# Kernel tuning notes

Hardware: AMD Instinct MI355X
Metric: run time of the kernel (lower is better)

Reference implementation:

```python
import jax, jax.numpy as jnp
import numpy as np

B, S, D = 4, 2048, 1024

def setup_inputs() -> dict:
    key = jax.random.key(0)
    k1, k2, k3, k4 = jax.random.split(key, 4)
    scale = 1.0 / np.sqrt(D)  # roughly glorot-like magnitude for weights
    return {
        "inputs": jax.random.normal(k1, (B, S, D), dtype=jnp.float32),
        "W_query": jax.random.normal(k2, (D, D), dtype=jnp.float32) * scale,
        "W_key": jax.random.normal(k3, (D, D), dtype=jnp.float32) * scale,
        "W_value": jax.random.normal(k4, (D, D), dtype=jnp.float32) * scale,
    }

def reference(inputs, W_query, W_key, W_value):
    # QKV projections: [B,S,D] @ [D,D]
    q = jnp.einsum('bsd,de->bse', inputs, W_query)
    k = jnp.einsum('bsd,de->bse', inputs, W_key)
    v = jnp.einsum('bsd,de->bse', inputs, W_value)
    # Unscaled attention scores [B,S,S] (source applies no 1/sqrt(d))
    score = jnp.einsum('bqd,bkd->bqk', q, k)
    weights = jax.nn.softmax(score, axis=-1)
    context = jnp.einsum('bqk,bkd->bqd', weights, v)
    return context
```

## Files before the change

### kernel.cpp

```cpp
#include <hip/hip_runtime.h>
#include <math.h>


typedef __bf16 bf16;
typedef _Float16 f16;
typedef __bf16 bf16x8 __attribute__((ext_vector_type(8)));
typedef __bf16 bf16x4 __attribute__((ext_vector_type(4)));
typedef _Float16 f16x4 __attribute__((ext_vector_type(4)));
typedef _Float16 f16x8 __attribute__((ext_vector_type(8)));
typedef float  f32x4  __attribute__((ext_vector_type(4)));

template<typename E> struct vec8_of;
template<> struct vec8_of<bf16> { using type = bf16x8; };
template<> struct vec8_of<f16>  { using type = f16x8; };

__device__ inline f32x4 mfma16(bf16x8 a, bf16x8 b, f32x4 c) {
    return __builtin_amdgcn_mfma_f32_16x16x32_bf16(a, b, c, 0, 0, 0);
}
__device__ inline f32x4 mfma16(f16x8 a, f16x8 b, f32x4 c) {
    return __builtin_amdgcn_mfma_f32_16x16x32_f16(a, b, c, 0, 0, 0);
}

#define AS1 __attribute__((address_space(1)))
#define AS3 __attribute__((address_space(3)))

template<typename E>
__device__ inline void async_load16(const E* g, void* l) {
    __builtin_amdgcn_global_load_lds((const AS1 unsigned int*)g,
                                     (AS3 unsigned int*)l, 16, 0, 0);
}

template<typename E, bool SPLIT, int OUT_MODE, int BK>
__device__ __forceinline__ void gemm_body(
    char* __restrict__ smraw,
    const E* __restrict__ Ahi, const E* __restrict__ Alo,
    const E* __restrict__ Bhi, const E* __restrict__ Blo,
    float* __restrict__ Cf, f16* __restrict__ Ch,
    int K, int lda, int ldb, int ldc,
    long long sA, long long sB, long long sC,
    int bx, int by, int bz)
{
    using vec8 = typename vec8_of<E>::type;
    constexpr int TILE_BYTES = 128 * BK * (int)sizeof(E);
    constexpr int CPW = (TILE_BYTES / 1024) / 4;
    constexpr int SPR = (BK * (int)sizeof(E)) / 16;
    constexpr int SWZ = (SPR == 8) ? 7 : 0;

    Ahi += (long long)bz * sA;
    Bhi += (long long)bz * sB;
    if (SPLIT) { Alo += (long long)bz * sA; Blo += (long long)bz * sB; }

    const int tid  = threadIdx.x;
    const int lane = tid & 63;
    const int wave = tid >> 6;
    const int quad = lane >> 4;
    const int l16  = lane & 15;
    const int wm   = (wave >> 1) * 64;
    const int wn   = (wave & 1) * 64;

    const long long rowA0 = (long long)by * 128;
    const long long colB0 = (long long)bx * 128;

    int ofs[CPW], rr[CPW], cc8[CPW];
#pragma unroll
    for (int u = 0; u < CPW; u++) {
        ofs[u] = (wave * CPW + u) * 1024 + lane * 16;
        const int s = ofs[u] >> 4;
        rr[u]  = s / SPR;
        cc8[u] = (s & (SPR - 1)) ^ (rr[u] & SWZ);
    }

    f32x4 acc[4][4];
#pragma unroll
    for (int i = 0; i < 4; i++)
#pragma unroll
        for (int j = 0; j < 4; j++) acc[i][j] = (f32x4){0.f, 0.f, 0.f, 0.f};

    for (int k0 = 0; k0 < K; k0 += BK) {
#pragma unroll
        for (int u = 0; u < CPW; u++) {
            async_load16(Ahi + (rowA0 + rr[u]) * lda + k0 + cc8[u] * 8, smraw + 0 * TILE_BYTES + ofs[u]);
            async_load16(Bhi + (colB0 + rr[u]) * ldb + k0 + cc8[u] * 8, smraw + 1 * TILE_BYTES + ofs[u]);
            if (SPLIT) {
                async_load16(Alo + (rowA0 + rr[u]) * lda + k0 + cc8[u] * 8, smraw + 2 * TILE_BYTES + ofs[u]);
                async_load16(Blo + (colB0 + rr[u]) * ldb + k0 + cc8[u] * 8, smraw + 3 * TILE_BYTES + ofs[u]);
            }
        }
        __syncthreads();

#pragma unroll
        for (int kh = 0; kh < BK / 32; kh++) {
            const int kc8 = kh * 4 + quad;
            vec8 a_hi[4], b_hi[4], a_lo[4], b_lo[4];
#pragma unroll
            for (int i = 0; i < 4; i++) {
                const int ra = wm + i * 16 + l16;
                const int rb = wn + i * 16 + l16;
                const int oa = ra * (SPR * 16) + ((kc8 ^ (ra & SWZ)) << 4);
                const int ob = rb * (SPR * 16) + ((kc8 ^ (rb & SWZ)) << 4);
                a_hi[i] = *(const vec8*)(smraw + 0 * TILE_BYTES + oa);
                b_hi[i] = *(const vec8*)(smraw + 1 * TILE_BYTES + ob);
                if (SPLIT) {
                    a_lo[i] = *(const vec8*)(smraw + 2 * TILE_BYTES + oa);
                    b_lo[i] = *(const vec8*)(smraw + 3 * TILE_BYTES + ob);
                }
            }
#pragma unroll
            for (int i = 0; i < 4; i++)
#pragma unroll
                for (int j = 0; j < 4; j++) {
                    acc[i][j] = mfma16(a_hi[i], b_hi[j], acc[i][j]);
                    if (SPLIT) {
                        acc[i][j] = mfma16(a_hi[i], b_lo[j], acc[i][j]);
                        acc[i][j] = mfma16(a_lo[i], b_hi[j], acc[i][j]);
                    }
                }
        }
        __syncthreads();
    }

    if (OUT_MODE == 2) {
        auto tr = (f16(*)[130])smraw;
#pragma unroll
        for (int i = 0; i < 4; i++)
#pragma unroll
            for (int j = 0; j < 4; j++)
#pragma unroll
                for (int e = 0; e < 4; e++)
                    tr[wn + j * 16 + l16][wm + i * 16 + quad * 4 + e] = (f16)acc[i][j][e];
        __syncthreads();
        const int batch = (int)(rowA0 >> 11);
        const int rib   = (int)(rowA0 & 2047);
        const int c  = tid >> 1;
        const int r0 = (tid & 1) << 6;
        f16* vt = Ch + (long long)batch * 1024 * 2048 + (long long)(colB0 + c) * ldc + rib + r0;
#pragma unroll
        for (int u = 0; u < 64; u += 8)
            *(f16x8*)(vt + u) = *(const f16x8*)&tr[c][r0 + u];
        return;
    }

    const long long cOff = (long long)bz * sC +
                           (rowA0 + wm + quad * 4) * (long long)ldc + colB0 + wn + l16;
#pragma unroll
    for (int i = 0; i < 4; i++)
#pragma unroll
        for (int e = 0; e < 4; e++) {
            const long long ro = cOff + (i * 16 + e) * ldc;
            if (OUT_MODE == 0) {
                float* rp = Cf + ro;
#pragma unroll
                for (int j = 0; j < 4; j++) rp[j * 16] = acc[i][j][e];
            } else {
                f16* rp = Ch + ro;
#pragma unroll
                for (int j = 0; j < 4; j++) rp[j * 16] = (f16)acc[i][j][e];
            }
        }
}

__global__ __launch_bounds__(256) void prep_all(
    const float4* __restrict__ X, f16* __restrict__ Xf,
    const float* __restrict__ Wq, const float* __restrict__ Wk, const float* __restrict__ Wv,
    bf16* __restrict__ Wq_h, bf16* __restrict__ Wq_l,
    bf16* __restrict__ Wk_h, bf16* __restrict__ Wk_l,
    f16* __restrict__ Wvt_f)
{
    int b = blockIdx.x;
    if (b < 8192) {
        long long i = (long long)b * 256 + threadIdx.x;
        float4 v = X[i];
        f16x4 fv = {(f16)v.x, (f16)v.y, (f16)v.z, (f16)v.w};
        *(f16x4*)(Xf + 4 * i) = fv;
    } else if (b < 10240) {
        const int b2 = b - 8192;
        const float4* W = (const float4*)(b2 < 1024 ? Wq : Wk);
        bf16* hh = b2 < 1024 ? Wq_h : Wk_h;
        bf16* ll = b2 < 1024 ? Wq_l : Wk_l;
        long long i = (long long)(b2 & 1023) * 256 + threadIdx.x;
        float4 v = W[i];
        bf16 a0 = (bf16)v.x, a1 = (bf16)v.y, a2 = (bf16)v.z, a3 = (bf16)v.w;
        bf16x4 hv = {a0, a1, a2, a3};
        bf16x4 lv = {(bf16)(v.x - (float)a0), (bf16)(v.y - (float)a1),
                     (bf16)(v.z - (float)a2), (bf16)(v.w - (float)a3)};
        *(bf16x4*)(hh + 4 * i) = hv;
        *(bf16x4*)(ll + 4 * i) = lv;
    } else {
        const int b3 = b - 10240;
        __shared__ float t[32][33];
        const int bx = (b3 & 31) * 32, by = (b3 >> 5) * 32;
        const int tx = threadIdx.x & 31, ty = threadIdx.x >> 5;
#pragma unroll
        for (int i = 0; i < 32; i += 8)
            t[ty + i][tx] = Wv[(long long)(by + ty + i) * 1024 + bx + tx];
        __syncthreads();
#pragma unroll
        for (int i = 0; i < 32; i += 8) {
            long long o = (long long)(bx + ty + i) * 1024 + by + tx;
            Wvt_f[o] = (f16)t[tx][ty + i];
        }
    }
}

__global__ __launch_bounds__(256) void tv_gemm(
    const f16* __restrict__ Xf, const f16* __restrict__ Mt_f,
    const f16* __restrict__ Wvt_f,
    f16* __restrict__ T, f16* __restrict__ Vt)
{
    extern __shared__ char smraw[];
    if (blockIdx.x < 8)
        gemm_body<f16, false, 1, 64>(smraw, Xf, nullptr, Mt_f, nullptr,
                                     nullptr, T, 1024, 1024, 1024, 1024,
                                     0, 0, 0, blockIdx.x, blockIdx.y, 0);
    else
        gemm_body<f16, false, 2, 64>(smraw, Xf, nullptr, Wvt_f, nullptr,
                                     nullptr, Vt, 1024, 1024, 1024, 2048,
                                     0, 0, 0, blockIdx.x - 8, blockIdx.y, 0);
}

template<typename E, bool SPLIT, int OUT_MODE, int BK>
__global__ __launch_bounds__(256) void gemm_bt(
    const E* __restrict__ Ahi, const E* __restrict__ Alo,
    const E* __restrict__ Bhi, const E* __restrict__ Blo,
    float* __restrict__ Cf, f16* __restrict__ Ch,
    int K, int lda, int ldb, int ldc,
    long long sA, long long sB, long long sC)
{
    extern __shared__ char smraw[];
    gemm_body<E, SPLIT, OUT_MODE, BK>(smraw, Ahi, Alo, Bhi, Blo, Cf, Ch,
                                      K, lda, ldb, ldc, sA, sB, sC,
                                      blockIdx.x, blockIdx.y, blockIdx.z);
}

__global__ __launch_bounds__(256) void softmax_f16(const float* __restrict__ S,
                                                   f16* __restrict__ P, int n)
{
    const long long row = blockIdx.x;
    const float* p = S + row * (long long)n;
    f16* q = P + row * (long long)n;
    const int tid = threadIdx.x;
    const int wv = tid >> 6, lane = tid & 63;

    float v[8];
    float m = -3.4e38f;
#pragma unroll
    for (int i = 0; i < 8; i++) { v[i] = p[tid + (i << 8)]; m = fmaxf(m, v[i]); }
#pragma unroll
    for (int off = 32; off > 0; off >>= 1) m = fmaxf(m, __shfl_xor(m, off, 64));

    __shared__ float red[4];
    if (lane == 0) red[wv] = m;
    __syncthreads();
    m = fmaxf(fmaxf(red[0], red[1]), fmaxf(red[2], red[3]));

    float s = 0.f;
#pragma unroll
    for (int i = 0; i < 8; i++) { v[i] = __expf(v[i] - m); s += v[i]; }
#pragma unroll
    for (int off = 32; off > 0; off >>= 1) s += __shfl_xor(s, off, 64);
    __syncthreads();
    if (lane == 0) red[wv] = s;
    __syncthreads();
    s = red[0] + red[1] + red[2] + red[3];

    const float inv = 1.0f / s;
#pragma unroll
    for (int i = 0; i < 8; i++) q[tid + (i << 8)] = (f16)(v[i] * inv);
}

extern "C" void kernel_launch(void* const* d_in, const int* in_sizes, int n_in,
                              void* d_out, int out_size, void* d_ws, size_t ws_size,
                              hipStream_t stream) {
    const float* X  = (const float*)d_in[0];
    const float* Wq = (const float*)d_in[1];
    const float* Wk = (const float*)d_in[2];
    const float* Wv = (const float*)d_in[3];
    float* out = (float*)d_out;

    char* w = (char*)d_ws;
    const long long MB = 1024LL * 1024;
    f16*  Xf    = (f16*) (w + 0 * MB);
    bf16* Wq_h  = (bf16*)(w + 16 * MB);
    bf16* Wq_l  = (bf16*)(w + 18 * MB);
    bf16* Wk_h  = (bf16*)(w + 20 * MB);
    bf16* Wk_l  = (bf16*)(w + 22 * MB);
    f16*  Wvt_f = (f16*) (w + 24 * MB);
    f16*  Mt_f  = (f16*) (w + 26 * MB);
    f16*  T     = (f16*) (w + 28 * MB);
    f16*  Vt    = (f16*) (w + 44 * MB);
    float* Sc   = (float*)(w + 60 * MB);
    f16*  P     = (f16*) (w + 124 * MB);

    dim3 blk(256);

    prep_all<<<dim3(11264), blk, 0, stream>>>(
        (const float4*)X, Xf, Wq, Wk, Wv, Wq_h, Wq_l, Wk_h, Wk_l, Wvt_f);

    gemm_bt<bf16, true, 1, 32><<<dim3(8, 8, 1), blk, 32768, stream>>>(
        Wk_h, Wk_l, Wq_h, Wq_l, nullptr, Mt_f,
        1024, 1024, 1024, 1024, 0, 0, 0);

    tv_gemm<<<dim3(16, 64, 1), blk, 33280, stream>>>(Xf, Mt_f, Wvt_f, T, Vt);

    gemm_bt<f16, false, 0, 64><<<dim3(16, 16, 4), blk, 32768, stream>>>(
        T, nullptr, Xf, nullptr, Sc, nullptr,
        1024, 1024, 1024, 2048,
        2048LL * 1024, 2048LL * 1024, 2048LL * 2048);

    softmax_f16<<<dim3(4 * 2048), blk, 0, stream>>>(Sc, P, 2048);

    gemm_bt<f16, false, 0, 64><<<dim3(8, 16, 4), blk, 32768, stream>>>(
        P, nullptr, Vt, nullptr, out, nullptr,
        2048, 2048, 2048, 1024,
        2048LL * 2048, 1024LL * 2048, 2048LL * 1024);
}
```

Measured before the change: 296.3 us.

## Fuse all attention stages into one cooperative persistent kernel with grid syncs

Replaces the sequence of six kernel launches with a single cooperative kernel of 1024 blocks that runs prep, the projection GEMMs, the score GEMM, softmax and the PV GEMM as phases separated by grid.sync(). It also splits the former fused tv_gemm into a Vt phase and a T phase. The aim is to remove per-launch overhead and inter-kernel gaps. In exchange the work is pinned to a fixed grid, and launch bounds of 4 blocks per CU may limit registers. Some phases leave blocks idle, and the original launch path is kept as a fallback if the cooperative launch fails.

```diff
diff --git a/kernel.cpp b/kernel.cpp
--- a/kernel.cpp
+++ b/kernel.cpp
@@ -1,5 +1,8 @@
 #include <hip/hip_runtime.h>
+#include <hip/hip_cooperative_groups.h>
 #include <math.h>
+
+namespace cg = cooperative_groups;
 
 
 typedef __bf16 bf16;
@@ -157,6 +160,141 @@
                 for (int j = 0; j < 4; j++) rp[j * 16] = (f16)acc[i][j][e];
             }
         }
+}
+
+__device__ __forceinline__ void prep_unit(
+    int u, int tid, char* smraw,
+    const float* __restrict__ X, f16* __restrict__ Xf,
+    const float* __restrict__ Wq, const float* __restrict__ Wk,
+    const float* __restrict__ Wv,
+    bf16* __restrict__ Wq_h, bf16* __restrict__ Wq_l,
+    bf16* __restrict__ Wk_h, bf16* __restrict__ Wk_l,
+    f16* __restrict__ Wvt_f)
+{
+    if (u < 8192) {
+        long long i = (long long)u * 256 + tid;
+        float4 v = ((const float4*)X)[i];
+        f16x4 fv = {(f16)v.x, (f16)v.y, (f16)v.z, (f16)v.w};
+        *(f16x4*)(Xf + 4 * i) = fv;
+    } else if (u < 10240) {
+        const int b2 = u - 8192;
+        const float4* W = (const float4*)(b2 < 1024 ? Wq : Wk);
+        bf16* hh = b2 < 1024 ? Wq_h : Wk_h;
+        bf16* ll = b2 < 1024 ? Wq_l : Wk_l;
+        long long i = (long long)(b2 & 1023) * 256 + tid;
+        float4 v = W[i];
+        bf16 a0 = (bf16)v.x, a1 = (bf16)v.y, a2 = (bf16)v.z, a3 = (bf16)v.w;
+        bf16x4 hv = {a0, a1, a2, a3};
+        bf16x4 lv = {(bf16)(v.x - (float)a0), (bf16)(v.y - (float)a1),
+                     (bf16)(v.z - (float)a2), (bf16)(v.w - (float)a3)};
+        *(bf16x4*)(hh + 4 * i) = hv;
+        *(bf16x4*)(ll + 4 * i) = lv;
+    } else {
+        const int b3 = u - 10240;
+        auto t = (float(*)[33])smraw;
+        const int bx = (b3 & 31) * 32, by = (b3 >> 5) * 32;
+        const int tx = tid & 31, ty = tid >> 5;
+#pragma unroll
+        for (int i = 0; i < 32; i += 8)
+            t[ty + i][tx] = Wv[(long long)(by + ty + i) * 1024 + bx + tx];
+        __syncthreads();
+#pragma unroll
+        for (int i = 0; i < 32; i += 8) {
+            long long o = (long long)(bx + ty + i) * 1024 + by + tx;
+            Wvt_f[o] = (f16)t[tx][ty + i];
+        }
+    }
+}
+
+__device__ __forceinline__ void softmax_row(
+    const float* __restrict__ S, f16* __restrict__ P,
+    long long row, int tid, char* smraw)
+{
+    float* red = (float*)smraw;
+    const float* p = S + row * 2048;
+    f16* q = P + row * 2048;
+    const int wv = tid >> 6, lane = tid & 63;
+
+    float v[8];
+    float m = -3.4e38f;
+#pragma unroll
+    for (int i = 0; i < 8; i++) { v[i] = p[tid + (i << 8)]; m = fmaxf(m, v[i]); }
+#pragma unroll
+    for (int off = 32; off > 0; off >>= 1) m = fmaxf(m, __shfl_xor(m, off, 64));
+
+    __syncthreads();
+    if (lane == 0) red[wv] = m;
+    __syncthreads();
+    m = fmaxf(fmaxf(red[0], red[1]), fmaxf(red[2], red[3]));
+
+    float s = 0.f;
+#pragma unroll
+    for (int i = 0; i < 8; i++) { v[i] = __expf(v[i] - m); s += v[i]; }
+#pragma unroll
+    for (int off = 32; off > 0; off >>= 1) s += __shfl_xor(s, off, 64);
+    __syncthreads();
+    if (lane == 0) red[wv] = s;
+    __syncthreads();
+    s = red[0] + red[1] + red[2] + red[3];
+
+    const float inv = 1.0f / s;
+#pragma unroll
+    for (int i = 0; i < 8; i++) q[tid + (i << 8)] = (f16)(v[i] * inv);
+}
+
+__global__ __launch_bounds__(256, 4) void attention_mega(
+    const float* __restrict__ X, const float* __restrict__ Wq,
+    const float* __restrict__ Wk, const float* __restrict__ Wv,
+    float* __restrict__ out, f16* __restrict__ Xf,
+    bf16* __restrict__ Wq_h, bf16* __restrict__ Wq_l,
+    bf16* __restrict__ Wk_h, bf16* __restrict__ Wk_l,
+    f16* __restrict__ Wvt_f, f16* __restrict__ Mt_f,
+    f16* __restrict__ T, f16* __restrict__ Vt,
+    float* __restrict__ Sc, f16* __restrict__ P)
+{
+    extern __shared__ char smraw[];
+    const int b   = blockIdx.x;
+    const int tid = threadIdx.x;
+    cg::grid_group grid = cg::this_grid();
+
+    for (int u = b; u < 11264; u += 1024)
+        prep_unit(u, tid, smraw, X, Xf, Wq, Wk, Wv,
+                  Wq_h, Wq_l, Wk_h, Wk_l, Wvt_f);
+    grid.sync();
+
+    if (b < 64) {
+        gemm_body<bf16, true, 1, 32>(smraw, Wk_h, Wk_l, Wq_h, Wq_l,
+                                     nullptr, Mt_f, 1024, 1024, 1024, 1024,
+                                     0, 0, 0, b & 7, b >> 3, 0);
+    } else if (b < 576) {
+        const int u = b - 64;
+        gemm_body<f16, false, 2, 64>(smraw, Xf, nullptr, Wvt_f, nullptr,
+                                     nullptr, Vt, 1024, 1024, 1024, 2048,
+                                     0, 0, 0, u & 7, u >> 3, 0);
+    }
+    grid.sync();
+
+    if (b < 512)
+        gemm_body<f16, false, 1, 64>(smraw, Xf, nullptr, Mt_f, nullptr,
+                                     nullptr, T, 1024, 1024, 1024, 1024,
+                                     0, 0, 0, b & 7, b >> 3, 0);
+    grid.sync();
+
+    gemm_body<f16, false, 0, 64>(smraw, T, nullptr, Xf, nullptr, Sc, nullptr,
+                                 1024, 1024, 1024, 2048,
+                                 2048LL * 1024, 2048LL * 1024, 2048LL * 2048,
+                                 b & 15, (b >> 4) & 15, b >> 8);
+    grid.sync();
+
+    for (int i = 0; i < 8; i++)
+        softmax_row(Sc, P, (long long)b * 8 + i, tid, smraw);
+    grid.sync();
+
+    if (b < 512)
+        gemm_body<f16, false, 0, 64>(smraw, P, nullptr, Vt, nullptr, out, nullptr,
+                                     2048, 2048, 2048, 1024,
+                                     2048LL * 2048, 1024LL * 2048, 2048LL * 1024,
+                                     b & 7, (b >> 3) & 15, b >> 7);
 }
 
 __global__ __launch_bounds__(256) void prep_all(
@@ -291,24 +429,28 @@
     float* Sc   = (float*)(w + 60 * MB);
     f16*  P     = (f16*) (w + 124 * MB);
 
+    void* kargs[] = { (void*)&X, (void*)&Wq, (void*)&Wk, (void*)&Wv,
+                      (void*)&out, (void*)&Xf,
+                      (void*)&Wq_h, (void*)&Wq_l, (void*)&Wk_h, (void*)&Wk_l,
+                      (void*)&Wvt_f, (void*)&Mt_f, (void*)&T, (void*)&Vt,
+                      (void*)&Sc, (void*)&P };
+    hipError_t err = hipLaunchCooperativeKernel(
+        reinterpret_cast<void*>(attention_mega),
+        dim3(1024), dim3(256), kargs, 33280, stream);
+    if (err == hipSuccess) return;
+
     dim3 blk(256);
-
     prep_all<<<dim3(11264), blk, 0, stream>>>(
         (const float4*)X, Xf, Wq, Wk, Wv, Wq_h, Wq_l, Wk_h, Wk_l, Wvt_f);
-
     gemm_bt<bf16, true, 1, 32><<<dim3(8, 8, 1), blk, 32768, stream>>>(
         Wk_h, Wk_l, Wq_h, Wq_l, nullptr, Mt_f,
         1024, 1024, 1024, 1024, 0, 0, 0);
-
     tv_gemm<<<dim3(16, 64, 1), blk, 33280, stream>>>(Xf, Mt_f, Wvt_f, T, Vt);
-
     gemm_bt<f16, false, 0, 64><<<dim3(16, 16, 4), blk, 32768, stream>>>(
         T, nullptr, Xf, nullptr, Sc, nullptr,
         1024, 1024, 1024, 2048,
         2048LL * 1024, 2048LL * 1024, 2048LL * 2048);
-
     softmax_f16<<<dim3(4 * 2048), blk, 0, stream>>>(Sc, P, 2048);
-
     gemm_bt<f16, false, 0, 64><<<dim3(8, 16, 4), blk, 32768, stream>>>(
         P, nullptr, Vt, nullptr, out, nullptr,
         2048, 2048, 2048, 1024,
```

New measurement: 863.4 us. 2.91x slower.

## Double-buffer f16 GEMM LDS tiles with BK=32 and vectorize softmax I/O

Applied to the files above, without the earlier changes.

Adds a double-buffered main loop for the f16 GEMMs. The next K-tile is issued via global_load_lds before computing on the current one, with explicit vmcnt waits and raw s_barrier instead of two __syncthreads per iteration. BK drops from 64 to 32 so two stages fit in the same LDS, and the swizzle for 4-slot rows changes to avoid bank conflicts. Softmax now uses float4 loads and f16x4 stores, which reassigns which columns each thread owns. The risks are more loop iterations with smaller tiles and hand-written waitcnt correctness.

```diff
diff --git a/kernel.cpp b/kernel.cpp
--- a/kernel.cpp
+++ b/kernel.cpp
@@ -30,7 +30,7 @@
                                      (AS3 unsigned int*)l, 16, 0, 0);
 }
 
-template<typename E, bool SPLIT, int OUT_MODE, int BK>
+template<typename E, bool SPLIT, int OUT_MODE, int BK, bool DBUF>
 __device__ __forceinline__ void gemm_body(
     char* __restrict__ smraw,
     const E* __restrict__ Ahi, const E* __restrict__ Alo,
@@ -44,7 +44,8 @@
     constexpr int TILE_BYTES = 128 * BK * (int)sizeof(E);
     constexpr int CPW = (TILE_BYTES / 1024) / 4;
     constexpr int SPR = (BK * (int)sizeof(E)) / 16;
-    constexpr int SWZ = (SPR == 8) ? 7 : 0;
+    constexpr int NMAT = SPLIT ? 4 : 2;
+    static_assert(!DBUF || (CPW == 2 && !SPLIT), "DBUF assumes 4 loads/stage");
 
     Ahi += (long long)bz * sA;
     Bhi += (long long)bz * sB;
@@ -61,13 +62,15 @@
     const long long rowA0 = (long long)by * 128;
     const long long colB0 = (long long)bx * 128;
 
+    auto swz = [](int r) -> int { return (SPR == 8) ? (r & 7) : ((r >> 1) & 3); };
+
     int ofs[CPW], rr[CPW], cc8[CPW];
 #pragma unroll
     for (int u = 0; u < CPW; u++) {
         ofs[u] = (wave * CPW + u) * 1024 + lane * 16;
         const int s = ofs[u] >> 4;
         rr[u]  = s / SPR;
-        cc8[u] = (s & (SPR - 1)) ^ (rr[u] & SWZ);
+        cc8[u] = (s & (SPR - 1)) ^ swz(rr[u]);
     }
 
     f32x4 acc[4][4];
@@ -76,18 +79,21 @@
 #pragma unroll
         for (int j = 0; j < 4; j++) acc[i][j] = (f32x4){0.f, 0.f, 0.f, 0.f};
 
-    for (int k0 = 0; k0 < K; k0 += BK) {
+    auto stage = [&](int k0, int buf) {
+        char* base = smraw + buf * (NMAT * TILE_BYTES);
 #pragma unroll
         for (int u = 0; u < CPW; u++) {
-            async_load16(Ahi + (rowA0 + rr[u]) * lda + k0 + cc8[u] * 8, smraw + 0 * TILE_BYTES + ofs[u]);
-            async_load16(Bhi + (colB0 + rr[u]) * ldb + k0 + cc8[u] * 8, smraw + 1 * TILE_BYTES + ofs[u]);
+            async_load16(Ahi + (rowA0 + rr[u]) * lda + k0 + cc8[u] * 8, base + 0 * TILE_BYTES + ofs[u]);
+            async_load16(Bhi + (colB0 + rr[u]) * ldb + k0 + cc8[u] * 8, base + 1 * TILE_BYTES + ofs[u]);
             if (SPLIT) {
-                async_load16(Alo + (rowA0 + rr[u]) * lda + k0 + cc8[u] * 8, smraw + 2 * TILE_BYTES + ofs[u]);
-                async_load16(Blo + (colB0 + rr[u]) * ldb + k0 + cc8[u] * 8, smraw + 3 * TILE_BYTES + ofs[u]);
+                async_load16(Alo + (rowA0 + rr[u]) * lda + k0 + cc8[u] * 8, base + 2 * TILE_BYTES + ofs[u]);
+                async_load16(Blo + (colB0 + rr[u]) * ldb + k0 + cc8[u] * 8, base + 3 * TILE_BYTES + ofs[u]);
             }
         }
-        __syncthreads();
-
+    };
+
+    auto compute = [&](int buf) {
+        char* base = smraw + buf * (NMAT * TILE_BYTES);
 #pragma unroll
         for (int kh = 0; kh < BK / 32; kh++) {
             const int kc8 = kh * 4 + quad;
@@ -96,13 +102,13 @@
             for (int i = 0; i < 4; i++) {
                 const int ra = wm + i * 16 + l16;
                 const int rb = wn + i * 16 + l16;
-                const int oa = ra * (SPR * 16) + ((kc8 ^ (ra & SWZ)) << 4);
-                const int ob = rb * (SPR * 16) + ((kc8 ^ (rb & SWZ)) << 4);
-                a_hi[i] = *(const vec8*)(smraw + 0 * TILE_BYTES + oa);
-                b_hi[i] = *(const vec8*)(smraw + 1 * TILE_BYTES + ob);
+                const int oa = ra * (SPR * 16) + ((kc8 ^ swz(ra)) << 4);
+                const int ob = rb * (SPR * 16) + ((kc8 ^ swz(rb)) << 4);
+                a_hi[i] = *(const vec8*)(base + 0 * TILE_BYTES + oa);
+                b_hi[i] = *(const vec8*)(base + 1 * TILE_BYTES + ob);
                 if (SPLIT) {
-                    a_lo[i] = *(const vec8*)(smraw + 2 * TILE_BYTES + oa);
-                    b_lo[i] = *(const vec8*)(smraw + 3 * TILE_BYTES + ob);
+                    a_lo[i] = *(const vec8*)(base + 2 * TILE_BYTES + oa);
+                    b_lo[i] = *(const vec8*)(base + 3 * TILE_BYTES + ob);
                 }
             }
 #pragma unroll
@@ -116,7 +122,34 @@
                     }
                 }
         }
-        __syncthreads();
+    };
+
+    if (DBUF) {
+        const int nt = K / BK;
+        stage(0, 0);
+        for (int t = 0; t < nt; t++) {
+            const int cur = t & 1;
+            if (t + 1 < nt) {
+                stage((t + 1) * BK, cur ^ 1);
+                asm volatile("s_waitcnt vmcnt(4)" ::: "memory");
+            } else {
+                asm volatile("s_waitcnt vmcnt(0)" ::: "memory");
+            }
+            __builtin_amdgcn_s_barrier();
+            asm volatile("" ::: "memory");
+            compute(cur);
+            asm volatile("s_waitcnt lgkmcnt(0)" ::: "memory");
+            __builtin_amdgcn_sched_barrier(0);
+            __builtin_amdgcn_s_barrier();
+            asm volatile("" ::: "memory");
+        }
+    } else {
+        for (int k0 = 0; k0 < K; k0 += BK) {
+            stage(k0, 0);
+            __syncthreads();
+            compute(0);
+            __syncthreads();
+        }
     }
 
     if (OUT_MODE == 2) {
@@ -209,16 +242,16 @@
 {
     extern __shared__ char smraw[];
     if (blockIdx.x < 8)
-        gemm_body<f16, false, 1, 64>(smraw, Xf, nullptr, Mt_f, nullptr,
-                                     nullptr, T, 1024, 1024, 1024, 1024,
-                                     0, 0, 0, blockIdx.x, blockIdx.y, 0);
+        gemm_body<f16, false, 1, 32, true>(smraw, Xf, nullptr, Mt_f, nullptr,
+                                           nullptr, T, 1024, 1024, 1024, 1024,
+                                           0, 0, 0, blockIdx.x, blockIdx.y, 0);
     else
-        gemm_body<f16, false, 2, 64>(smraw, Xf, nullptr, Wvt_f, nullptr,
-                                     nullptr, Vt, 1024, 1024, 1024, 2048,
-                                     0, 0, 0, blockIdx.x - 8, blockIdx.y, 0);
-}
-
-template<typename E, bool SPLIT, int OUT_MODE, int BK>
+        gemm_body<f16, false, 2, 32, true>(smraw, Xf, nullptr, Wvt_f, nullptr,
+                                           nullptr, Vt, 1024, 1024, 1024, 2048,
+                                           0, 0, 0, blockIdx.x - 8, blockIdx.y, 0);
+}
+
+template<typename E, bool SPLIT, int OUT_MODE, int BK, bool DBUF>
 __global__ __launch_bounds__(256) void gemm_bt(
     const E* __restrict__ Ahi, const E* __restrict__ Alo,
     const E* __restrict__ Bhi, const E* __restrict__ Blo,
@@ -227,24 +260,25 @@
     long long sA, long long sB, long long sC)
 {
     extern __shared__ char smraw[];
-    gemm_body<E, SPLIT, OUT_MODE, BK>(smraw, Ahi, Alo, Bhi, Blo, Cf, Ch,
-                                      K, lda, ldb, ldc, sA, sB, sC,
-                                      blockIdx.x, blockIdx.y, blockIdx.z);
+    gemm_body<E, SPLIT, OUT_MODE, BK, DBUF>(smraw, Ahi, Alo, Bhi, Blo, Cf, Ch,
+                                            K, lda, ldb, ldc, sA, sB, sC,
+                                            blockIdx.x, blockIdx.y, blockIdx.z);
 }
 
 __global__ __launch_bounds__(256) void softmax_f16(const float* __restrict__ S,
                                                    f16* __restrict__ P, int n)
 {
     const long long row = blockIdx.x;
-    const float* p = S + row * (long long)n;
+    const float4* p = (const float4*)(S + row * (long long)n);
     f16* q = P + row * (long long)n;
     const int tid = threadIdx.x;
     const int wv = tid >> 6, lane = tid & 63;
 
-    float v[8];
+    float4 va = p[tid], vb = p[tid + 256];
+    float v[8] = {va.x, va.y, va.z, va.w, vb.x, vb.y, vb.z, vb.w};
     float m = -3.4e38f;
 #pragma unroll
-    for (int i = 0; i < 8; i++) { v[i] = p[tid + (i << 8)]; m = fmaxf(m, v[i]); }
+    for (int i = 0; i < 8; i++) m = fmaxf(m, v[i]);
 #pragma unroll
     for (int off = 32; off > 0; off >>= 1) m = fmaxf(m, __shfl_xor(m, off, 64));
 
@@ -264,8 +298,10 @@
     s = red[0] + red[1] + red[2] + red[3];
 
     const float inv = 1.0f / s;
-#pragma unroll
-    for (int i = 0; i < 8; i++) q[tid + (i << 8)] = (f16)(v[i] * inv);
+    f16x4 o0 = {(f16)(v[0] * inv), (f16)(v[1] * inv), (f16)(v[2] * inv), (f16)(v[3] * inv)};
+    f16x4 o1 = {(f16)(v[4] * inv), (f16)(v[5] * inv), (f16)(v[6] * inv), (f16)(v[7] * inv)};
+    *(f16x4*)(q + tid * 4) = o0;
+    *(f16x4*)(q + 1024 + tid * 4) = o1;
 }
 
 extern "C" void kernel_launch(void* const* d_in, const int* in_sizes, int n_in,
@@ -296,20 +332,20 @@
     prep_all<<<dim3(11264), blk, 0, stream>>>(
         (const float4*)X, Xf, Wq, Wk, Wv, Wq_h, Wq_l, Wk_h, Wk_l, Wvt_f);
 
-    gemm_bt<bf16, true, 1, 32><<<dim3(8, 8, 1), blk, 32768, stream>>>(
+    gemm_bt<bf16, true, 1, 32, false><<<dim3(8, 8, 1), blk, 32768, stream>>>(
         Wk_h, Wk_l, Wq_h, Wq_l, nullptr, Mt_f,
         1024, 1024, 1024, 1024, 0, 0, 0);
 
     tv_gemm<<<dim3(16, 64, 1), blk, 33280, stream>>>(Xf, Mt_f, Wvt_f, T, Vt);
 
-    gemm_bt<f16, false, 0, 64><<<dim3(16, 16, 4), blk, 32768, stream>>>(
+    gemm_bt<f16, false, 0, 32, true><<<dim3(16, 16, 4), blk, 32768, stream>>>(
         T, nullptr, Xf, nullptr, Sc, nullptr,
         1024, 1024, 1024, 2048,
         2048LL * 1024, 2048LL * 1024, 2048LL * 2048);
 
     softmax_f16<<<dim3(4 * 2048), blk, 0, stream>>>(Sc, P, 2048);
 
-    gemm_bt<f16, false, 0, 64><<<dim3(8, 16, 4), blk, 32768, stream>>>(
+    gemm_bt<f16, false, 0, 32, true><<<dim3(8, 16, 4), blk, 32768, stream>>>(
         P, nullptr, Vt, nullptr, out, nullptr,
         2048, 2048, 2048, 1024,
         2048LL * 2048, 1024LL * 2048, 2048LL * 1024);
```

After: 302.8 us. 1.02x slower.

## Add 256x256-tile 8-wave pipelined f16 GEMM for projection and attention GEMMs

Applied to the files above, without the earlier changes.

Adds a new GEMM kernel with 256x256 output tiles, 512 threads (8 waves) and a double-buffered LDS pipeline. It splits the B tile into halves and interleaves async global-to-LDS loads with MFMA phases, using explicit waitcnt, barriers and setprio. The kernel replaces the 128x128 GEMMs for the T/Vt projections, the score GEMM and the PV GEMM, aiming for more data reuse per tile and overlap of loads with compute. The softmax is vectorised to float4 loads and f16x4 stores, and the old split-precision GEMM gets a different swizzle for BK=32. Trade-offs: fewer blocks than there are CUs on some grids (e.g. 128 blocks for PV), and heavier register pressure.

```diff
diff --git a/kernel.cpp b/kernel.cpp
--- a/kernel.cpp
+++ b/kernel.cpp
@@ -28,6 +28,193 @@
 __device__ inline void async_load16(const E* g, void* l) {
     __builtin_amdgcn_global_load_lds((const AS1 unsigned int*)g,
                                      (AS3 unsigned int*)l, 16, 0, 0);
+}
+
+#define SBAR()  do { __builtin_amdgcn_s_barrier(); __builtin_amdgcn_sched_barrier(0); } while (0)
+#define WAITV(n) do { asm volatile("s_waitcnt vmcnt(" #n ")" ::: "memory"); __builtin_amdgcn_sched_barrier(0); } while (0)
+#define WAITL() do { asm volatile("s_waitcnt lgkmcnt(0)" ::: "memory"); __builtin_amdgcn_sched_barrier(0); } while (0)
+
+template<int OUT_MODE>
+__device__ __forceinline__ void gemm8_body(
+    char* __restrict__ smraw,
+    const f16* __restrict__ A, const f16* __restrict__ B,
+    float* __restrict__ Cf, f16* __restrict__ Ch,
+    int K, int lda, int ldb, int ldc,
+    long long sA, long long sB, long long sC,
+    int bx, int by, int bz)
+{
+    A += (long long)bz * sA;
+    B += (long long)bz * sB;
+
+    const int tid  = threadIdx.x;
+    const int lane = tid & 63;
+    const int wave = tid >> 6;
+    const int quad = lane >> 4;
+    const int l16  = lane & 15;
+    const int wm   = wave >> 2;
+    const int wn   = wave & 3;
+
+    const long long rowA0 = (long long)by * 256;
+    const long long colB0 = (long long)bx * 256;
+
+    const int s0 = tid, s1 = 512 + tid;
+    const int aRow0 = s0 >> 2, aRow1 = s1 >> 2;
+    const int aCol0 = ((s0 & 3) ^ ((s0 >> 4) & 3)) * 8;
+    const int aCol1 = ((s1 & 3) ^ ((s1 >> 4) & 3)) * 8;
+    const int ci    = s0 >> 2;
+    const int bRow0 = (ci >> 5) * 64 + (ci & 31);
+    const int bCol  = aCol0;
+
+    const f16* aSrc0 = A + (rowA0 + aRow0) * lda + aCol0;
+    const f16* aSrc1 = A + (rowA0 + aRow1) * lda + aCol1;
+    const f16* b0Src = B + (colB0 + bRow0) * ldb + bCol;
+    const f16* b1Src = b0Src + 32LL * ldb;
+
+    const int dA0 = tid * 16, dA1 = 8192 + tid * 16, dB = tid * 16;
+
+    const int nt = K >> 5;
+
+    auto stageA = [&](int t) {
+        char* buf = smraw + ((t & 1) << 15);
+        async_load16(aSrc0 + t * 32, buf + dA0);
+        async_load16(aSrc1 + t * 32, buf + dA1);
+    };
+    auto stageB0 = [&](int t) {
+        char* buf = smraw + ((t & 1) << 15);
+        async_load16(b0Src + t * 32, buf + 16384 + dB);
+    };
+    auto stageB1 = [&](int t) {
+        char* buf = smraw + ((t & 1) << 15);
+        async_load16(b1Src + t * 32, buf + 24576 + dB);
+    };
+
+    const int lofs = l16 * 64 + ((quad ^ ((l16 >> 2) & 3)) << 4);
+    const int aoff = wm * 8192 + lofs;
+    const int boff = wn * 2048 + lofs;
+
+    f32x4 acc[8][4];
+#pragma unroll
+    for (int i = 0; i < 8; i++)
+#pragma unroll
+        for (int j = 0; j < 4; j++) acc[i][j] = (f32x4){0.f, 0.f, 0.f, 0.f};
+
+    stageA(0); stageB0(0); stageB1(0);
+    stageA(1); stageB0(1);
+    WAITV(4);
+    SBAR();
+
+    for (int t = 0; t < nt; t++) {
+        const char* buf = smraw + ((t & 1) << 15);
+        f16x8 av[8], bv[2];
+
+#pragma unroll
+        for (int i = 0; i < 8; i++) av[i] = *(const f16x8*)(buf + aoff + i * 1024);
+#pragma unroll
+        for (int j = 0; j < 2; j++) bv[j] = *(const f16x8*)(buf + 16384 + boff + j * 1024);
+        if (t + 1 < nt) stageB1(t + 1);
+        SBAR();
+        WAITL();
+        __builtin_amdgcn_s_setprio(1);
+#pragma unroll
+        for (int i = 0; i < 8; i++) {
+            acc[i][0] = mfma16(av[i], bv[0], acc[i][0]);
+            acc[i][1] = mfma16(av[i], bv[1], acc[i][1]);
+        }
+        __builtin_amdgcn_s_setprio(0);
+        if (t + 1 < nt) { WAITV(4); } else { WAITV(0); }
+        SBAR();
+
+#pragma unroll
+        for (int j = 0; j < 2; j++) bv[j] = *(const f16x8*)(buf + 24576 + boff + j * 1024);
+        if (t + 2 < nt) { stageA(t + 2); stageB0(t + 2); }
+        SBAR();
+        WAITL();
+        __builtin_amdgcn_s_setprio(1);
+#pragma unroll
+        for (int i = 0; i < 8; i++) {
+            acc[i][2] = mfma16(av[i], bv[0], acc[i][2]);
+            acc[i][3] = mfma16(av[i], bv[1], acc[i][3]);
+        }
+        __builtin_amdgcn_s_setprio(0);
+        if (t + 2 < nt) { WAITV(4); }
+        else if (t + 1 < nt) { WAITV(1); }
+        SBAR();
+    }
+
+    if (OUT_MODE == 2) {
+        auto tr = (f16(*)[72])smraw;
+        const int batch = (int)(rowA0 >> 11);
+        const long long rib = rowA0 & 2047;
+        const int c  = tid >> 1;
+        const int r0 = (tid & 1) << 5;
+#pragma unroll
+        for (int h = 0; h < 2; h++)
+#pragma unroll
+            for (int iq = 0; iq < 2; iq++) {
+                __syncthreads();
+                if (wm == h) {
+#pragma unroll
+                    for (int i2 = 0; i2 < 4; i2++)
+#pragma unroll
+                        for (int j = 0; j < 4; j++)
+#pragma unroll
+                            for (int e = 0; e < 4; e++)
+                                tr[wn * 64 + j * 16 + l16][i2 * 16 + quad * 4 + e] =
+                                    (f16)acc[iq * 4 + i2][j][e];
+                }
+                __syncthreads();
+                f16* vt = Ch + (long long)batch * 1024 * 2048 +
+                          (long long)(colB0 + c) * ldc + rib + h * 128 + iq * 64 + r0;
+#pragma unroll
+                for (int u = 0; u < 32; u += 8)
+                    *(f16x8*)(vt + u) = *(const f16x8*)&tr[c][r0 + u];
+            }
+        return;
+    }
+
+    const long long cOff = (long long)bz * sC +
+                           (rowA0 + wm * 128 + quad * 4) * (long long)ldc +
+                           colB0 + wn * 64 + l16;
+#pragma unroll
+    for (int i = 0; i < 8; i++)
+#pragma unroll
+        for (int e = 0; e < 4; e++) {
+            const long long ro = cOff + (long long)(i * 16 + e) * ldc;
+            if (OUT_MODE == 0) {
+                float* rp = Cf + ro;
+#pragma unroll
+                for (int j = 0; j < 4; j++) rp[j * 16] = acc[i][j][e];
+            } else {
+                f16* rp = Ch + ro;
+#pragma unroll
+                for (int j = 0; j < 4; j++) rp[j * 16] = (f16)acc[i][j][e];
+            }
+        }
+}
+
+__global__ __launch_bounds__(512, 2) void tv8(
+    const f16* __restrict__ Xf, const f16* __restrict__ Mt_f,
+    const f16* __restrict__ Wvt_f, f16* __restrict__ T, f16* __restrict__ Vt)
+{
+    extern __shared__ char smraw[];
+    if (blockIdx.x < 4)
+        gemm8_body<1>(smraw, Xf, Mt_f, nullptr, T, 1024, 1024, 1024, 1024,
+                      0, 0, 0, blockIdx.x, blockIdx.y, 0);
+    else
+        gemm8_body<2>(smraw, Xf, Wvt_f, nullptr, Vt, 1024, 1024, 1024, 2048,
+                      0, 0, 0, blockIdx.x - 4, blockIdx.y, 0);
+}
+
+template<int OUT_MODE>
+__global__ __launch_bounds__(512, 2) void gemm8_k(
+    const f16* __restrict__ A, const f16* __restrict__ B,
+    float* __restrict__ Cf, f16* __restrict__ Ch,
+    int K, int lda, int ldb, int ldc,
+    long long sA, long long sB, long long sC)
+{
+    extern __shared__ char smraw[];
+    gemm8_body<OUT_MODE>(smraw, A, B, Cf, Ch, K, lda, ldb, ldc, sA, sB, sC,
+                         blockIdx.x, blockIdx.y, blockIdx.z);
 }
 
 template<typename E, bool SPLIT, int OUT_MODE, int BK>
@@ -44,7 +231,6 @@
     constexpr int TILE_BYTES = 128 * BK * (int)sizeof(E);
     constexpr int CPW = (TILE_BYTES / 1024) / 4;
     constexpr int SPR = (BK * (int)sizeof(E)) / 16;
-    constexpr int SWZ = (SPR == 8) ? 7 : 0;
 
     Ahi += (long long)bz * sA;
     Bhi += (long long)bz * sB;
@@ -61,13 +247,15 @@
     const long long rowA0 = (long long)by * 128;
     const long long colB0 = (long long)bx * 128;
 
+    auto swz = [](int r) -> int { return (SPR == 8) ? (r & 7) : ((r >> 1) & 3); };
+
     int ofs[CPW], rr[CPW], cc8[CPW];
 #pragma unroll
     for (int u = 0; u < CPW; u++) {
         ofs[u] = (wave * CPW + u) * 1024 + lane * 16;
         const int s = ofs[u] >> 4;
         rr[u]  = s / SPR;
-        cc8[u] = (s & (SPR - 1)) ^ (rr[u] & SWZ);
+        cc8[u] = (s & (SPR - 1)) ^ swz(rr[u]);
     }
 
     f32x4 acc[4][4];
@@ -96,8 +284,8 @@
             for (int i = 0; i < 4; i++) {
                 const int ra = wm + i * 16 + l16;
                 const int rb = wn + i * 16 + l16;
-                const int oa = ra * (SPR * 16) + ((kc8 ^ (ra & SWZ)) << 4);
-                const int ob = rb * (SPR * 16) + ((kc8 ^ (rb & SWZ)) << 4);
+                const int oa = ra * (SPR * 16) + ((kc8 ^ swz(ra)) << 4);
+                const int ob = rb * (SPR * 16) + ((kc8 ^ swz(rb)) << 4);
                 a_hi[i] = *(const vec8*)(smraw + 0 * TILE_BYTES + oa);
                 b_hi[i] = *(const vec8*)(smraw + 1 * TILE_BYTES + ob);
                 if (SPLIT) {
@@ -119,27 +307,6 @@
         __syncthreads();
     }
 
-    if (OUT_MODE == 2) {
-        auto tr = (f16(*)[130])smraw;
-#pragma unroll
-        for (int i = 0; i < 4; i++)
-#pragma unroll
-            for (int j = 0; j < 4; j++)
-#pragma unroll
-                for (int e = 0; e < 4; e++)
-                    tr[wn + j * 16 + l16][wm + i * 16 + quad * 4 + e] = (f16)acc[i][j][e];
-        __syncthreads();
-        const int batch = (int)(rowA0 >> 11);
-        const int rib   = (int)(rowA0 & 2047);
-        const int c  = tid >> 1;
-        const int r0 = (tid & 1) << 6;
-        f16* vt = Ch + (long long)batch * 1024 * 2048 + (long long)(colB0 + c) * ldc + rib + r0;
-#pragma unroll
-        for (int u = 0; u < 64; u += 8)
-            *(f16x8*)(vt + u) = *(const f16x8*)&tr[c][r0 + u];
-        return;
-    }
-
     const long long cOff = (long long)bz * sC +
                            (rowA0 + wm + quad * 4) * (long long)ldc + colB0 + wn + l16;
 #pragma unroll
@@ -157,6 +324,20 @@
                 for (int j = 0; j < 4; j++) rp[j * 16] = (f16)acc[i][j][e];
             }
         }
+}
+
+template<typename E, bool SPLIT, int OUT_MODE, int BK>
+__global__ __launch_bounds__(256) void gemm_bt(
+    const E* __restrict__ Ahi, const E* __restrict__ Alo,
+    const E* __restrict__ Bhi, const E* __restrict__ Blo,
+    float* __restrict__ Cf, f16* __restrict__ Ch,
+    int K, int lda, int ldb, int ldc,
+    long long sA, long long sB, long long sC)
+{
+    extern __shared__ char smraw[];
+    gemm_body<E, SPLIT, OUT_MODE, BK>(smraw, Ahi, Alo, Bhi, Blo, Cf, Ch,
+                                      K, lda, ldb, ldc, sA, sB, sC,
+                                      blockIdx.x, blockIdx.y, blockIdx.z);
 }
 
 __global__ __launch_bounds__(256) void prep_all(
@@ -202,49 +383,20 @@
     }
 }
 
-__global__ __launch_bounds__(256) void tv_gemm(
-    const f16* __restrict__ Xf, const f16* __restrict__ Mt_f,
-    const f16* __restrict__ Wvt_f,
-    f16* __restrict__ T, f16* __restrict__ Vt)
-{
-    extern __shared__ char smraw[];
-    if (blockIdx.x < 8)
-        gemm_body<f16, false, 1, 64>(smraw, Xf, nullptr, Mt_f, nullptr,
-                                     nullptr, T, 1024, 1024, 1024, 1024,
-                                     0, 0, 0, blockIdx.x, blockIdx.y, 0);
-    else
-        gemm_body<f16, false, 2, 64>(smraw, Xf, nullptr, Wvt_f, nullptr,
-                                     nullptr, Vt, 1024, 1024, 1024, 2048,
-                                     0, 0, 0, blockIdx.x - 8, blockIdx.y, 0);
-}
-
-template<typename E, bool SPLIT, int OUT_MODE, int BK>
-__global__ __launch_bounds__(256) void gemm_bt(
-    const E* __restrict__ Ahi, const E* __restrict__ Alo,
-    const E* __restrict__ Bhi, const E* __restrict__ Blo,
-    float* __restrict__ Cf, f16* __restrict__ Ch,
-    int K, int lda, int ldb, int ldc,
-    long long sA, long long sB, long long sC)
-{
-    extern __shared__ char smraw[];
-    gemm_body<E, SPLIT, OUT_MODE, BK>(smraw, Ahi, Alo, Bhi, Blo, Cf, Ch,
-                                      K, lda, ldb, ldc, sA, sB, sC,
-                                      blockIdx.x, blockIdx.y, blockIdx.z);
-}
-
 __global__ __launch_bounds__(256) void softmax_f16(const float* __restrict__ S,
                                                    f16* __restrict__ P, int n)
 {
     const long long row = blockIdx.x;
-    const float* p = S + row * (long long)n;
+    const float4* p = (const float4*)(S + row * (long long)n);
     f16* q = P + row * (long long)n;
     const int tid = threadIdx.x;
     const int wv = tid >> 6, lane = tid & 63;
 
-    float v[8];
+    float4 va = p[tid], vb = p[tid + 256];
+    float v[8] = {va.x, va.y, va.z, va.w, vb.x, vb.y, vb.z, vb.w};
     float m = -3.4e38f;
 #pragma unroll
-    for (int i = 0; i < 8; i++) { v[i] = p[tid + (i << 8)]; m = fmaxf(m, v[i]); }
+    for (int i = 0; i < 8; i++) m = fmaxf(m, v[i]);
 #pragma unroll
     for (int off = 32; off > 0; off >>= 1) m = fmaxf(m, __shfl_xor(m, off, 64));
 
@@ -264,8 +416,10 @@
     s = red[0] + red[1] + red[2] + red[3];
 
     const float inv = 1.0f / s;
-#pragma unroll
-    for (int i = 0; i < 8; i++) q[tid + (i << 8)] = (f16)(v[i] * inv);
+    f16x4 o0 = {(f16)(v[0] * inv), (f16)(v[1] * inv), (f16)(v[2] * inv), (f16)(v[3] * inv)};
+    f16x4 o1 = {(f16)(v[4] * inv), (f16)(v[5] * inv), (f16)(v[6] * inv), (f16)(v[7] * inv)};
+    *(f16x4*)(q + tid * 4) = o0;
+    *(f16x4*)(q + 1024 + tid * 4) = o1;
 }
 
 extern "C" void kernel_launch(void* const* d_in, const int* in_sizes, int n_in,
@@ -300,17 +454,15 @@
         Wk_h, Wk_l, Wq_h, Wq_l, nullptr, Mt_f,
         1024, 1024, 1024, 1024, 0, 0, 0);
 
-    tv_gemm<<<dim3(16, 64, 1), blk, 33280, stream>>>(Xf, Mt_f, Wvt_f, T, Vt);
-
-    gemm_bt<f16, false, 0, 64><<<dim3(16, 16, 4), blk, 32768, stream>>>(
-        T, nullptr, Xf, nullptr, Sc, nullptr,
-        1024, 1024, 1024, 2048,
+    tv8<<<dim3(8, 32), dim3(512), 65536, stream>>>(Xf, Mt_f, Wvt_f, T, Vt);
+
+    gemm8_k<0><<<dim3(8, 8, 4), dim3(512), 65536, stream>>>(
+        T, Xf, Sc, nullptr, 1024, 1024, 1024, 2048,
         2048LL * 1024, 2048LL * 1024, 2048LL * 2048);
 
     softmax_f16<<<dim3(4 * 2048), blk, 0, stream>>>(Sc, P, 2048);
 
-    gemm_bt<f16, false, 0, 64><<<dim3(8, 16, 4), blk, 32768, stream>>>(
-        P, nullptr, Vt, nullptr, out, nullptr,
-        2048, 2048, 2048, 1024,
+    gemm8_k<0><<<dim3(4, 8, 4), dim3(512), 65536, stream>>>(
+        P, Vt, out, nullptr, 2048, 2048, 2048, 1024,
         2048LL * 2048, 1024LL * 2048, 2048LL * 1024);
 }
```

After: 313.2 us. 1.06x slower.
